# Optimization experiments

Measured on AMD Instinct MI355X. Metric: run time of the kernel, lower is better.

The kernel has to match this reference:

```python
import jax, jax.numpy as jnp
import numpy as np
import math

B, S, D_MODEL, N_HEADS = 4, 2048, 1024, 16
D_HEAD = D_MODEL // N_HEADS

def _xavier(key, shape, gain):
    # nn.init.xavier_uniform_ on [n_heads, fan_in, fan_out]: fan from last two dims
    fan_in, fan_out = shape[-2], shape[-1]
    bound = gain * math.sqrt(6.0 / (fan_in + fan_out))
    return jax.random.uniform(key, shape, jnp.float32, -bound, bound)

def setup_inputs() -> dict:
    key = jax.random.key(0)
    ks = jax.random.split(key, 5)
    g = 1.0 / math.sqrt(2.0)
    return {
        "x": jax.random.normal(ks[0], (B, S, D_MODEL), jnp.float32),
        "W_Q": _xavier(ks[1], (N_HEADS, D_MODEL, D_HEAD), g),
        "W_K": _xavier(ks[2], (N_HEADS, D_MODEL, D_HEAD), g),
        "W_V": _xavier(ks[3], (N_HEADS, D_MODEL, D_HEAD), g),
        "W_O": _xavier(ks[4], (N_HEADS, D_HEAD, D_MODEL), 1.0),
        "b_Q": jnp.zeros((N_HEADS, D_HEAD), jnp.float32),
        "b_K": jnp.zeros((N_HEADS, D_HEAD), jnp.float32),
        "b_V": jnp.zeros((N_HEADS, D_HEAD), jnp.float32),
        "b_O": jnp.zeros((D_MODEL,), jnp.float32),
    }

def reference(x, W_Q, W_K, W_V, W_O, b_Q, b_K, b_V, b_O):
    # q,k,v: [b, s, h, d_head]
    q = jnp.einsum('bsd,hde->bshe', x, W_Q) + b_Q
    k = jnp.einsum('bsd,hde->bshe', x, W_K) + b_K
    v = jnp.einsum('bsd,hde->bshe', x, W_V) + b_V
    scores = jnp.einsum('bqhe,bkhe->bhqk', q, k) / jnp.sqrt(jnp.float32(D_HEAD))
    attn = jax.nn.softmax(scores, axis=-1)  # [b, h, q, k]
    v_out = jnp.einsum('bkhe,bhqk->bqhe', v, attn)
    return jnp.einsum('bqhe,hed->bqd', v_out, W_O) + b_O
```

## Files before the change

### kernel.cpp

```cpp
#include <hip/hip_runtime.h>
#include <hip/hip_bf16.h>
#include <cmath>

#define B_ 4
#define S_ 2048
#define DM_ 1024
#define H_ 16
#define DH_ 64
#define BS_ (B_*S_)

typedef __bf16 bf16x8 __attribute__((ext_vector_type(8)));
typedef __bf16 bf16x4 __attribute__((ext_vector_type(4)));
typedef float  floatx4 __attribute__((ext_vector_type(4)));

__device__ __forceinline__ void gl_lds16(const __bf16* g, __bf16* l) {
  __builtin_amdgcn_global_load_lds(
      (const __attribute__((address_space(1))) void*)g,
      (__attribute__((address_space(3))) void*)l, 16, 0, 0);
}

__global__ void transpose_kernel(const float* __restrict__ src, __bf16* __restrict__ dst,
                                 int R, int C, long srcBatch, long dstBatch) {
  __shared__ __bf16 tile[32][33];
  int b = blockIdx.z;
  long sb = (long)b * srcBatch;
  dst += (long)b * dstBatch;
  int c0 = blockIdx.x * 32, r0 = blockIdx.y * 32;
  int tx = threadIdx.x, ty = threadIdx.y;
  #pragma unroll
  for (int i = 0; i < 32; i += 8)
    tile[ty + i][tx] = (__bf16)src[sb + (long)(r0 + ty + i) * C + (c0 + tx)];
  __syncthreads();
  #pragma unroll
  for (int i = 0; i < 32; i += 8)
    dst[(long)(c0 + ty + i) * R + (r0 + tx)] = tile[tx][ty + i];
}

__global__ void cvt_kernel(const float* __restrict__ src, __bf16* __restrict__ dst) {
  long i = ((long)blockIdx.x * 256 + threadIdx.x) * 8;
  float4 a = *(const float4*)(src + i);
  float4 b = *(const float4*)(src + i + 4);
  bf16x8 t;
  t[0] = (__bf16)a.x; t[1] = (__bf16)a.y; t[2] = (__bf16)a.z; t[3] = (__bf16)a.w;
  t[4] = (__bf16)b.x; t[5] = (__bf16)b.y; t[6] = (__bf16)b.z; t[7] = (__bf16)b.w;
  *(bf16x8*)(dst + i) = t;
}

#define BM 128
#define BN 128
#define BK 64

template<int EPI>
__global__ __launch_bounds__(256, 2) void gemm_kernel(
    const __bf16* __restrict__ A, const __bf16* __restrict__ Bt,
    int M, int N, int K,
    const float* __restrict__ bq, const float* __restrict__ bk,
    const float* __restrict__ bv, const float* __restrict__ bo,
    __bf16* __restrict__ q_ws, __bf16* __restrict__ k_ws,
    __bf16* __restrict__ vT_ws, float* __restrict__ out) {

  __shared__ __align__(16) __bf16 As[2][BM * BK];
  __shared__ __align__(16) __bf16 Bs[2][BN * BK];

  int tid  = threadIdx.x;
  int wave = tid >> 6, lane = tid & 63;
  int quad = lane >> 4, l15 = lane & 15;
  int wm = (wave >> 1) * 64, wn = (wave & 1) * 64;

  int nbx = gridDim.x;
  int lid = blockIdx.y * nbx + blockIdx.x;
  int cpx = (nbx * gridDim.y) >> 3;
  int sid = (lid & 7) * cpx + (lid >> 3);
  long m0 = (long)(sid / nbx) * BM;
  long n0 = (long)(sid % nbx) * BN;

  floatx4 acc[4][4] = {};

  int r  = tid >> 3, c8 = tid & 7;
  int cx = c8 ^ (r & 7);
  const __bf16* Asrc = A  + (m0 + r) * (long)K + cx * 8;
  const __bf16* Bsrc = Bt + (n0 + r) * (long)K + cx * 8;

#define STAGE(buf, k0) do {                                                  \
    _Pragma("unroll")                                                        \
    for (int i = 0; i < 4; i++) {                                            \
      gl_lds16(Asrc + (long)(i * 32) * K + (k0), &As[buf][(i * 256 + tid) * 8]); \
      gl_lds16(Bsrc + (long)(i * 32) * K + (k0), &Bs[buf][(i * 256 + tid) * 8]); \
    }                                                                        \
  } while (0)

  int swz = l15 & 7;
  const int NT = K / BK;

  STAGE(0, 0);

  for (int t = 0; t < NT; ++t) {
    int cur = t & 1;
    __syncthreads();
    if (t + 1 < NT) STAGE(cur ^ 1, (t + 1) * BK);

    #pragma unroll
    for (int kk = 0; kk < 2; kk++) {
      bf16x8 af[4], bff[4];
      #pragma unroll
      for (int mt = 0; mt < 4; mt++)
        af[mt] = *(const bf16x8*)(&As[cur][(wm + mt * 16 + l15) * 64 + (((kk * 4 + quad) ^ swz) * 8)]);
      #pragma unroll
      for (int nt = 0; nt < 4; nt++)
        bff[nt] = *(const bf16x8*)(&Bs[cur][(wn + nt * 16 + l15) * 64 + (((kk * 4 + quad) ^ swz) * 8)]);
      #pragma unroll
      for (int mt = 0; mt < 4; mt++)
        #pragma unroll
        for (int nt = 0; nt < 4; nt++)
          acc[mt][nt] = __builtin_amdgcn_mfma_f32_16x16x32_bf16(af[mt], bff[nt], acc[mt][nt], 0, 0, 0);
    }
  }
#undef STAGE

  if (EPI == 0) {
    #pragma unroll
    for (int nt = 0; nt < 4; nt++) {
      long n = n0 + wn + nt * 16 + l15;
      int seg = (int)(n >> 10);
      int he  = (int)(n & 1023);
      int h = he >> 6, e = he & 63;
      const float* bias = (seg == 0 ? bq : (seg == 1 ? bk : bv));
      float bval = bias[he];
      float scale = (seg == 0 ? 0.125f * 1.44269504088896340f : 1.0f);
      #pragma unroll
      for (int mt = 0; mt < 4; mt++) {
        #pragma unroll
        for (int rr = 0; rr < 4; rr++) {
          long m = m0 + wm + mt * 16 + quad * 4 + rr;
          int b = (int)(m >> 11), s = (int)(m & 2047);
          float v = (acc[mt][nt][rr] + bval) * scale;
          if (seg == 0)
            q_ws[((long)(b * 16 + h) * 2048 + s) * 64 + e] = (__bf16)v;
          else if (seg == 1)
            k_ws[((long)(b * 16 + h) * 2048 + s) * 64 + e] = (__bf16)v;
          else
            vT_ws[((long)(b * 16 + h) * 64 + e) * 2048 + s] = (__bf16)v;
        }
      }
    }
  } else {
    #pragma unroll
    for (int mt = 0; mt < 4; mt++) {
      #pragma unroll
      for (int rr = 0; rr < 4; rr++) {
        long m = m0 + wm + mt * 16 + quad * 4 + rr;
        #pragma unroll
        for (int nt = 0; nt < 4; nt++) {
          long n = n0 + wn + nt * 16 + l15;
          out[m * N + n] = acc[mt][nt][rr] + bo[n];
        }
      }
    }
  }
}

#define KBLK 64

__global__ __launch_bounds__(256, 4) void attn_kernel(
    const __bf16* __restrict__ Q, const __bf16* __restrict__ Kk,
    const __bf16* __restrict__ Vt, __bf16* __restrict__ vout) {

  __shared__ __align__(16) __bf16 Kb[2][64 * 64];
  __shared__ __align__(16) __bf16 Vb[2][64 * 64];
  __shared__ __align__(16) __bf16 Pb[4][16 * 64];

  int tid = threadIdx.x, wave = tid >> 6, lane = tid & 63;
  int quad = lane >> 4, l15 = lane & 15;

  int id = blockIdx.x;
  int xcd = id & 7, rest = id >> 3;
  int qt = rest & 15, bhhi = rest >> 4;
  int bh = bhhi * 8 + xcd;
  int b = bh >> 4, h = bh & 15;
  int q0 = qt * 128 + wave * 32;

  const __bf16* Qbh = Q  + (long)(b * 16 + h) * 2048 * 64;
  const __bf16* Kbh = Kk + (long)(b * 16 + h) * 2048 * 64;
  const __bf16* Vbh = Vt + (long)(b * 16 + h) * 64 * 2048;

  int rs0 = tid >> 3, cc0 = tid & 7;
  int ccs = cc0 ^ (rs0 & 7);
  const __bf16* Ksrc0 = Kbh + (long)rs0 * 64 + ccs * 8;
  const __bf16* Ksrc1 = Kbh + (long)(rs0 + 32) * 64 + ccs * 8;
  const __bf16* Vsrc0 = Vbh + (long)rs0 * 2048 + ccs * 8;
  const __bf16* Vsrc1 = Vbh + (long)(rs0 + 32) * 2048 + ccs * 8;

#define STAGE(buf, kb) do {                                   \
    gl_lds16(Ksrc0 + (long)(kb) * 64, &Kb[buf][tid * 8]);      \
    gl_lds16(Ksrc1 + (long)(kb) * 64, &Kb[buf][tid * 8 + 2048]); \
    gl_lds16(Vsrc0 + (kb),            &Vb[buf][tid * 8]);      \
    gl_lds16(Vsrc1 + (kb),            &Vb[buf][tid * 8 + 2048]); \
  } while (0)

  bf16x8 qf[2][2];
  #pragma unroll
  for (int qh = 0; qh < 2; qh++)
    #pragma unroll
    for (int t = 0; t < 2; t++)
      qf[qh][t] = *(const bf16x8*)(Qbh + (long)(q0 + qh * 16 + l15) * 64 + t * 32 + quad * 8);

  floatx4 o[2][4] = {};
  floatx4 ol[2] = {};
  bf16x8 onesv;
  #pragma unroll
  for (int j = 0; j < 8; j++) onesv[j] = (__bf16)1.0f;

  int swz = l15 & 7;

  STAGE(0, 0);

  for (int kb = 0; kb < 2048; kb += KBLK) {
    int cur = (kb >> 6) & 1;

    __syncthreads();
    if (kb + KBLK < 2048) STAGE(cur ^ 1, kb + KBLK);

    floatx4 sc[2][4];
    __builtin_amdgcn_s_setprio(1);
    #pragma unroll
    for (int nt = 0; nt < 4; nt++) {
      const __bf16* kp = &Kb[cur][(nt * 16 + l15) * 64];
      bf16x8 k0 = *(const bf16x8*)(kp + ((0 + quad) ^ swz) * 8);
      bf16x8 k1 = *(const bf16x8*)(kp + ((4 + quad) ^ swz) * 8);
      #pragma unroll
      for (int qh = 0; qh < 2; qh++) {
        floatx4 z = { 0.f, 0.f, 0.f, 0.f };
        z = __builtin_amdgcn_mfma_f32_16x16x32_bf16(k0, qf[qh][0], z, 0, 0, 0);
        sc[qh][nt] = __builtin_amdgcn_mfma_f32_16x16x32_bf16(k1, qf[qh][1], z, 0, 0, 0);
      }
    }
    __builtin_amdgcn_s_setprio(0);

    #pragma unroll
    for (int qh = 0; qh < 2; qh++) {
      #pragma unroll
      for (int nt = 0; nt < 4; nt++) {
        bf16x4 pw;
        #pragma unroll
        for (int rr = 0; rr < 4; rr++)
          pw[rr] = (__bf16)__builtin_amdgcn_exp2f(sc[qh][nt][rr]);
        *(bf16x4*)(&Pb[wave][l15 * 64 + (((nt * 2 + (quad >> 1)) ^ swz) * 8) + (quad & 1) * 4]) = pw;
      }

      __builtin_amdgcn_s_setprio(1);
      #pragma unroll
      for (int t = 0; t < 2; t++) {
        bf16x8 pf = *(const bf16x8*)(&Pb[wave][l15 * 64 + ((t * 4 + quad) ^ swz) * 8]);
        ol[qh] = __builtin_amdgcn_mfma_f32_16x16x32_bf16(onesv, pf, ol[qh], 0, 0, 0);
        #pragma unroll
        for (int dn = 0; dn < 4; dn++) {
          bf16x8 vf = *(const bf16x8*)(&Vb[cur][(dn * 16 + l15) * 64 + ((t * 4 + quad) ^ swz) * 8]);
          o[qh][dn] = __builtin_amdgcn_mfma_f32_16x16x32_bf16(vf, pf, o[qh][dn], 0, 0, 0);
        }
      }
      __builtin_amdgcn_s_setprio(0);
    }
  }
#undef STAGE

  #pragma unroll
  for (int qh = 0; qh < 2; qh++) {
    float rl = 1.f / ol[qh][0];
    int s = q0 + qh * 16 + l15;
    __bf16* outr = vout + ((long)(b * 2048 + s) * 16 + h) * 64;
    #pragma unroll
    for (int dn = 0; dn < 4; dn++) {
      bf16x4 w;
      #pragma unroll
      for (int rr = 0; rr < 4; rr++) w[rr] = (__bf16)(o[qh][dn][rr] * rl);
      *(bf16x4*)(outr + dn * 16 + quad * 4) = w;
    }
  }
}

extern "C" void kernel_launch(void* const* d_in, const int* in_sizes, int n_in,
                              void* d_out, int out_size, void* d_ws, size_t ws_size,
                              hipStream_t stream) {
  const float* x  = (const float*)d_in[0];
  const float* WQ = (const float*)d_in[1];
  const float* WK = (const float*)d_in[2];
  const float* WV = (const float*)d_in[3];
  const float* WO = (const float*)d_in[4];
  const float* bq = (const float*)d_in[5];
  const float* bk = (const float*)d_in[6];
  const float* bv = (const float*)d_in[7];
  const float* bo = (const float*)d_in[8];
  float* out = (float*)d_out;

  uint8_t* ws = (uint8_t*)d_ws;
  const long MB16 = 16777216;
  __bf16* q_ws  = (__bf16*)(ws);
  __bf16* k_ws  = (__bf16*)(ws + 1 * MB16);
  __bf16* vT_ws = (__bf16*)(ws + 2 * MB16);
  __bf16* Wt    = (__bf16*)(ws + 3 * MB16);
  __bf16* vout  = (__bf16*)(ws + 3 * MB16);
  __bf16* WOt   = (__bf16*)(ws);
  __bf16* xb    = (__bf16*)d_out;

  dim3 tb(32, 8);
  transpose_kernel<<<dim3(2, 32, 16), tb, 0, stream>>>(WQ, Wt,               1024, 64, 65536, 65536);
  transpose_kernel<<<dim3(2, 32, 16), tb, 0, stream>>>(WK, Wt + 1024 * 1024, 1024, 64, 65536, 65536);
  transpose_kernel<<<dim3(2, 32, 16), tb, 0, stream>>>(WV, Wt + 2048 * 1024, 1024, 64, 65536, 65536);

  cvt_kernel<<<dim3(4096), 256, 0, stream>>>(x, xb);

  gemm_kernel<0><<<dim3(3072 / BN, 8192 / BM), 256, 0, stream>>>(
      xb, Wt, BS_, 3072, DM_, bq, bk, bv, nullptr, q_ws, k_ws, vT_ws, nullptr);

  attn_kernel<<<dim3(1024), 256, 0, stream>>>(q_ws, k_ws, vT_ws, vout);

  transpose_kernel<<<dim3(32, 32, 1), tb, 0, stream>>>(WO, WOt, 1024, 1024, 0, 0);

  gemm_kernel<1><<<dim3(1024 / BN, 8192 / BM), 256, 0, stream>>>(
      vout, WOt, BS_, DM_, DM_, nullptr, nullptr, nullptr, bo, nullptr, nullptr, nullptr, out);
}
```

Before: 295.1 us.

## Single-buffer GEMM LDS for higher occupancy and stage V transpose through LDS

Replaces the double-buffered A/B shared-memory tiles with one buffer, which halves LDS use, and raises launch bounds from 2 to 4 blocks per CU. The next tile is now loaded after compute, behind an extra barrier, so global-to-LDS loads no longer overlap the MFMA work within a block; the bet is that extra resident blocks hide that latency instead. The QKV epilogue now branches once per block on segment, and the V segment is transposed through LDS so vT can be written as contiguous 16-byte stores instead of scattered 2-byte ones. Forcing 4 blocks per CU may cap registers per thread and cause spills of the 64-float accumulator.

After: 267.7 us. 9.3% less time.

```diff
diff --git a/kernel.cpp b/kernel.cpp
--- a/kernel.cpp
+++ b/kernel.cpp
@@ -51,7 +51,7 @@
 #define BK 64
 
 template<int EPI>
-__global__ __launch_bounds__(256, 2) void gemm_kernel(
+__global__ __launch_bounds__(256, 4) void gemm_kernel(
     const __bf16* __restrict__ A, const __bf16* __restrict__ Bt,
     int M, int N, int K,
     const float* __restrict__ bq, const float* __restrict__ bk,
@@ -59,8 +59,9 @@
     __bf16* __restrict__ q_ws, __bf16* __restrict__ k_ws,
     __bf16* __restrict__ vT_ws, float* __restrict__ out) {
 
-  __shared__ __align__(16) __bf16 As[2][BM * BK];
-  __shared__ __align__(16) __bf16 Bs[2][BN * BK];
+  __shared__ __align__(16) __bf16 smem[17408];
+  __bf16* As = smem;
+  __bf16* Bs = smem + 8192;
 
   int tid  = threadIdx.x;
   int wave = tid >> 6, lane = tid & 63;
@@ -81,66 +82,96 @@
   const __bf16* Asrc = A  + (m0 + r) * (long)K + cx * 8;
   const __bf16* Bsrc = Bt + (n0 + r) * (long)K + cx * 8;
 
-#define STAGE(buf, k0) do {                                                  \
+#define STAGE(k0) do {                                                       \
     _Pragma("unroll")                                                        \
     for (int i = 0; i < 4; i++) {                                            \
-      gl_lds16(Asrc + (long)(i * 32) * K + (k0), &As[buf][(i * 256 + tid) * 8]); \
-      gl_lds16(Bsrc + (long)(i * 32) * K + (k0), &Bs[buf][(i * 256 + tid) * 8]); \
+      gl_lds16(Asrc + (long)(i * 32) * K + (k0), &As[(i * 256 + tid) * 8]);  \
+      gl_lds16(Bsrc + (long)(i * 32) * K + (k0), &Bs[(i * 256 + tid) * 8]);  \
     }                                                                        \
   } while (0)
 
   int swz = l15 & 7;
   const int NT = K / BK;
 
-  STAGE(0, 0);
+  STAGE(0);
 
   for (int t = 0; t < NT; ++t) {
-    int cur = t & 1;
     __syncthreads();
-    if (t + 1 < NT) STAGE(cur ^ 1, (t + 1) * BK);
 
     #pragma unroll
     for (int kk = 0; kk < 2; kk++) {
       bf16x8 af[4], bff[4];
       #pragma unroll
       for (int mt = 0; mt < 4; mt++)
-        af[mt] = *(const bf16x8*)(&As[cur][(wm + mt * 16 + l15) * 64 + (((kk * 4 + quad) ^ swz) * 8)]);
+        af[mt] = *(const bf16x8*)(&As[(wm + mt * 16 + l15) * 64 + (((kk * 4 + quad) ^ swz) * 8)]);
       #pragma unroll
       for (int nt = 0; nt < 4; nt++)
-        bff[nt] = *(const bf16x8*)(&Bs[cur][(wn + nt * 16 + l15) * 64 + (((kk * 4 + quad) ^ swz) * 8)]);
+        bff[nt] = *(const bf16x8*)(&Bs[(wn + nt * 16 + l15) * 64 + (((kk * 4 + quad) ^ swz) * 8)]);
       #pragma unroll
       for (int mt = 0; mt < 4; mt++)
         #pragma unroll
         for (int nt = 0; nt < 4; nt++)
           acc[mt][nt] = __builtin_amdgcn_mfma_f32_16x16x32_bf16(af[mt], bff[nt], acc[mt][nt], 0, 0, 0);
     }
+
+    if (t + 1 < NT) {
+      __syncthreads();
+      STAGE((t + 1) * BK);
+    }
   }
 #undef STAGE
 
   if (EPI == 0) {
-    #pragma unroll
-    for (int nt = 0; nt < 4; nt++) {
-      long n = n0 + wn + nt * 16 + l15;
-      int seg = (int)(n >> 10);
-      int he  = (int)(n & 1023);
-      int h = he >> 6, e = he & 63;
-      const float* bias = (seg == 0 ? bq : (seg == 1 ? bk : bv));
-      float bval = bias[he];
-      float scale = (seg == 0 ? 0.125f * 1.44269504088896340f : 1.0f);
-      #pragma unroll
-      for (int mt = 0; mt < 4; mt++) {
-        #pragma unroll
-        for (int rr = 0; rr < 4; rr++) {
-          long m = m0 + wm + mt * 16 + quad * 4 + rr;
-          int b = (int)(m >> 11), s = (int)(m & 2047);
-          float v = (acc[mt][nt][rr] + bval) * scale;
-          if (seg == 0)
-            q_ws[((long)(b * 16 + h) * 2048 + s) * 64 + e] = (__bf16)v;
-          else if (seg == 1)
-            k_ws[((long)(b * 16 + h) * 2048 + s) * 64 + e] = (__bf16)v;
-          else
-            vT_ws[((long)(b * 16 + h) * 64 + e) * 2048 + s] = (__bf16)v;
+    int seg = (int)(n0 >> 10);
+    if (seg < 2) {
+      #pragma unroll
+      for (int nt = 0; nt < 4; nt++) {
+        long n = n0 + wn + nt * 16 + l15;
+        int he  = (int)(n & 1023);
+        int h = he >> 6, e = he & 63;
+        const float* bias = (seg == 0 ? bq : bk);
+        float bval = bias[he];
+        float scale = (seg == 0 ? 0.125f * 1.44269504088896340f : 1.0f);
+        __bf16* dst0 = (seg == 0 ? q_ws : k_ws);
+        #pragma unroll
+        for (int mt = 0; mt < 4; mt++) {
+          #pragma unroll
+          for (int rr = 0; rr < 4; rr++) {
+            long m = m0 + wm + mt * 16 + quad * 4 + rr;
+            int b = (int)(m >> 11), s = (int)(m & 2047);
+            float v = (acc[mt][nt][rr] + bval) * scale;
+            dst0[((long)(b * 16 + h) * 2048 + s) * 64 + e] = (__bf16)v;
+          }
         }
+      }
+    } else {
+      __syncthreads();
+      __bf16* vl = smem + wave * 4352;
+      #pragma unroll
+      for (int nt = 0; nt < 4; nt++) {
+        long n = n0 + wn + nt * 16 + l15;
+        float bval = bv[(int)(n & 1023)];
+        #pragma unroll
+        for (int mt = 0; mt < 4; mt++) {
+          bf16x4 pw;
+          #pragma unroll
+          for (int rr = 0; rr < 4; rr++) pw[rr] = (__bf16)(acc[mt][nt][rr] + bval);
+          *(bf16x4*)(&vl[(nt * 16 + l15) * 68 + mt * 16 + quad * 4]) = pw;
+        }
+      }
+      asm volatile("s_waitcnt lgkmcnt(0)" ::: "memory");
+      int bb = (int)((m0 + wm) >> 11), s0 = (int)((m0 + wm) & 2047);
+      #pragma unroll
+      for (int rep = 0; rep < 2; rep++) {
+        int j = (lane >> 1) + rep * 32;
+        long n = n0 + wn + j;
+        int he = (int)(n & 1023);
+        int h = he >> 6, e = he & 63;
+        __bf16* dst = vT_ws + ((long)(bb * 16 + h) * 64 + e) * 2048 + s0 + (lane & 1) * 32;
+        const __bf16* srcl = &vl[j * 68 + (lane & 1) * 32];
+        #pragma unroll
+        for (int c = 0; c < 4; c++)
+          *(bf16x8*)(dst + c * 8) = *(const bf16x8*)(srcl + c * 8);
       }
     }
   } else {
```
